# Performance work log

Measured on AMD Instinct MI355X. Metric: run time of the kernel, lower is better.

Reference implementation:

```python
import jax, jax.numpy as jnp
import numpy as np

N = 50000          # num nodes
DEG = 16           # constant out-degree -> edges[:,0] sorted, every node present
E = N * DEG
NODE_IN = 128
NODE_OUT = 64
EDGE_IN = 128
EDGE_OUT = 64      # must equal NODE_OUT for the reshape in the original module


def _xavier_uniform(key, shape):
    fan_in, fan_out = shape[0], shape[1]
    a = np.sqrt(6.0 / (fan_in + fan_out)).astype(np.float32)
    return jax.random.uniform(key, shape, jnp.float32, -a, a)


def setup_inputs() -> dict:
    key = jax.random.key(0)
    k1, k2, k3, k4, k5, k6, k7 = jax.random.split(key, 7)
    node_fts = jax.random.normal(k1, (N, NODE_IN), jnp.float32)
    edge_fts = jax.random.normal(k2, (N, EDGE_IN), jnp.float32)
    # sorted sources with constant degree so unique(src).shape[0] == N and
    # the original's repeat(bincount) trick is equivalent to gather-by-src
    src = jnp.repeat(jnp.arange(N, dtype=jnp.int32), DEG)
    dst = jax.random.randint(k3, (E,), 0, N, dtype=jnp.int32)
    edges = jnp.stack([src, dst], axis=1)  # [E, 2]
    W_node = _xavier_uniform(k4, (NODE_IN, NODE_OUT))
    W_edge = _xavier_uniform(k5, (EDGE_IN, EDGE_OUT))
    a_node = _xavier_uniform(k6, (2 * NODE_OUT, 1))
    a_edge = _xavier_uniform(k7, (NODE_OUT + EDGE_OUT, 1))
    return {"node_fts": node_fts, "edge_fts": edge_fts, "edges": edges,
            "W_node": W_node, "W_edge": W_edge,
            "a_node": a_node, "a_edge": a_edge}


def reference(node_fts, edge_fts, edges, W_node, W_edge, a_node, a_edge):
    src = edges[:, 0]
    h_v = node_fts @ W_node            # [N, NODE_OUT]
    e_v = edge_fts @ W_edge            # [N, EDGE_OUT]

    # gather endpoint features -> [E, 2*NODE_OUT] / [E, NODE_OUT+EDGE_OUT]
    h_pair = h_v[edges].reshape(-1, 2 * NODE_OUT)
    e_pair = e_v[edges].reshape(-1, NODE_OUT + EDGE_OUT)

    leaky = lambda x: jnp.where(x > 0, x, 0.2 * x)
    node_att = leaky((h_pair @ a_node)[:, 0])   # [E]
    edge_att = leaky((e_pair @ a_edge)[:, 0])   # [E]

    node_att = jnp.exp(jnp.clip(node_att, -2.0, 2.0))
    edge_att = jnp.exp(jnp.clip(edge_att, -2.0, 2.0))

    node_sum = jax.ops.segment_sum(node_att, src, num_segments=N)
    edge_sum = jax.ops.segment_sum(edge_att, src, num_segments=N)

    node_att_norm = node_att / node_sum[src]
    edge_att_norm = edge_att / edge_sum[src]

    node_att_var = jnp.var(node_att_norm, ddof=1)  # torch.var is unbiased
    edge_att_var = jnp.var(edge_att_norm, ddof=1)

    node_out = jax.ops.segment_sum(h_pair * node_att_norm[:, None], src, num_segments=N)
    edge_out = jax.ops.segment_sum(e_pair * edge_att_norm[:, None], src, num_segments=N)
    return node_out, edge_out, node_att_var, edge_att_var
```

## Files before the change

### kernel.cpp

```cpp
#include <hip/hip_runtime.h>
#include <hip/hip_bf16.h>

#define NN 50000
#define DEG 16
#define EE (NN*DEG)
#define CHUNKS 3125

typedef unsigned int uint;
typedef __attribute__((ext_vector_type(8))) short bf16x8;
typedef __attribute__((ext_vector_type(4))) float f32x4;

__device__ inline unsigned short f2b(float f){
  uint u = __float_as_uint(f);
  uint r = (u + 0x7FFFu + ((u >> 16) & 1u)) >> 16;
  return (unsigned short)r;
}
__device__ inline float b2f(uint lo16){ return __uint_as_float(lo16 << 16); }

__global__ __launch_bounds__(256) void gemm_mfma_kernel(
    const float* __restrict__ in0, const float* __restrict__ in1,
    const float* __restrict__ W0,  const float* __restrict__ W1,
    const float* __restrict__ a0,  const float* __restrict__ a1,
    unsigned short* __restrict__ hev,
    float* __restrict__ s1ne, float* __restrict__ s2ne)
{
  const int pass = blockIdx.y;
  const float* in   = pass ? in1 : in0;
  const float* W    = pass ? W1  : W0;
  const float* av   = pass ? a1  : a0;

  __shared__ unsigned short Wt[64*128];
  const int tid = threadIdx.x;
  for (int b = tid; b < 1024; b += 256) {
    const int n  = b >> 4;
    const int k0 = (b & 15) * 8;
    uint4 pk;
    unsigned short* ps = (unsigned short*)&pk;
    #pragma unroll
    for (int j = 0; j < 8; j++) ps[j] = f2b(W[(k0 + j)*64 + n]);
    const int byte = n*256 + ((k0*2) ^ ((n & 7) << 4));
    *(uint4*)((char*)Wt + byte) = pk;
  }
  __syncthreads();

  const int wv   = tid >> 6;
  const int lane = tid & 63;
  const int g    = lane >> 4;
  const int c    = lane & 15;

  bf16x8 wfrag[4][4];
  #pragma unroll
  for (int kt = 0; kt < 4; kt++) {
    #pragma unroll
    for (int nt = 0; nt < 4; nt++) {
      const int n  = nt*16 + c;
      const int kb = (kt*32 + g*8) * 2;
      const int byte = n*256 + (kb ^ ((n & 7) << 4));
      wfrag[kt][nt] = *(bf16x8*)((char*)Wt + byte);
    }
  }
  float a1r[4], a2r[4];
  #pragma unroll
  for (int t = 0; t < 4; t++) { a1r[t] = av[t*16 + c]; a2r[t] = av[64 + t*16 + c]; }

  for (int ch = blockIdx.x*4 + wv; ch < CHUNKS; ch += gridDim.x*4) {
    const int r0 = ch * 16;
    const float* rowp = in + (long)(r0 + c)*128 + g*8;
    float4 ald[8];
    #pragma unroll
    for (int kt = 0; kt < 4; kt++) {
      ald[kt*2]   = *(const float4*)(rowp + kt*32);
      ald[kt*2+1] = *(const float4*)(rowp + kt*32 + 4);
    }
    f32x4 acc[4];
    #pragma unroll
    for (int nt = 0; nt < 4; nt++) acc[nt] = (f32x4){0.f, 0.f, 0.f, 0.f};
    #pragma unroll
    for (int kt = 0; kt < 4; kt++) {
      const float4 u = ald[kt*2], w = ald[kt*2+1];
      bf16x8 af;
      af[0] = (short)f2b(u.x); af[1] = (short)f2b(u.y);
      af[2] = (short)f2b(u.z); af[3] = (short)f2b(u.w);
      af[4] = (short)f2b(w.x); af[5] = (short)f2b(w.y);
      af[6] = (short)f2b(w.z); af[7] = (short)f2b(w.w);
      #pragma unroll
      for (int nt = 0; nt < 4; nt++)
        acc[nt] = __builtin_amdgcn_mfma_f32_16x16x32_bf16(af, wfrag[kt][nt], acc[nt], 0, 0, 0);
    }
    float q1v[4], q2v[4];
    #pragma unroll
    for (int v = 0; v < 4; v++) {
      float t1 = 0.f, t2 = 0.f;
      #pragma unroll
      for (int nt = 0; nt < 4; nt++) {
        t1 = fmaf(acc[nt][v], a1r[nt], t1);
        t2 = fmaf(acc[nt][v], a2r[nt], t2);
      }
      #pragma unroll
      for (int off = 1; off < 16; off <<= 1) {
        t1 += __shfl_xor(t1, off);
        t2 += __shfl_xor(t2, off);
      }
      q1v[v] = t1; q2v[v] = t2;
    }
    if (c < 4) {
      const float sv1 = (c==0) ? q1v[0] : (c==1) ? q1v[1] : (c==2) ? q1v[2] : q1v[3];
      const float sv2 = (c==0) ? q2v[0] : (c==1) ? q2v[1] : (c==2) ? q2v[2] : q2v[3];
      const int r = r0 + g*4 + c;
      s1ne[(long)r*2 + pass] = sv1;
      s2ne[(long)r*2 + pass] = sv2;
    }
    #pragma unroll
    for (int nt = 0; nt < 4; nt++) {
      #pragma unroll
      for (int v = 0; v < 4; v++) {
        const long r = r0 + g*4 + v;
        hev[r*128 + pass*64 + nt*16 + c] = f2b(acc[nt][v]);
      }
    }
  }
}

__global__ __launch_bounds__(256) void attn_kernel(
    const uint* __restrict__ hev,
    const float2* __restrict__ s1ne, const float2* __restrict__ s2ne,
    const int* __restrict__ edges,
    float* __restrict__ outp, double* __restrict__ partials)
{
  const int tid  = threadIdx.x;
  const int wv   = tid >> 6;
  const int lane = tid & 63;
  const int j    = lane >> 4;
  const int cc   = lane & 31;
  double a_qn = 0.0, a_qe = 0.0;
  float* node_out = outp;
  float* edge_out = outp + (long)NN*128;
  const int NG = NN/4;
  for (int grp = blockIdx.x*4 + wv; grp < NG; grp += gridDim.x*4) {
    const int i0 = grp*4;
    const int dst = edges[((long)i0*16 + lane)*2 + 1];
    const float2 s1v = s1ne[i0 + j];
    const float2 gsc = s2ne[dst];
    float xn = s1v.x + gsc.x;
    float xe = s1v.y + gsc.y;
    xn = xn > 0.f ? xn : 0.2f*xn;
    xe = xe > 0.f ? xe : 0.2f*xe;
    xn = fminf(fmaxf(xn, -2.f), 2.f);
    xe = fminf(fmaxf(xe, -2.f), 2.f);
    const float an = expf(xn);
    const float ae = expf(xe);
    float sn = an, se = ae;
    #pragma unroll
    for (int off = 1; off < 16; off <<= 1) {
      sn += __shfl_xor(sn, off);
      se += __shfl_xor(se, off);
    }
    const float wn = an / sn;
    const float we = ae / se;
    float rq = wn*wn, re = we*we;
    #pragma unroll
    for (int off = 1; off < 64; off <<= 1) {
      rq += __shfl_xor(rq, off);
      re += __shfl_xor(re, off);
    }
    if (lane == 0) { a_qn += (double)rq; a_qe += (double)re; }
    float acc0[4], acc1[4];
    #pragma unroll
    for (int t = 0; t < 4; t++) { acc0[t] = 0.f; acc1[t] = 0.f; }
    #pragma unroll
    for (int k = 0; k < 64; k++) {
      const int d     = __builtin_amdgcn_readlane(dst, k);
      const float wnk = __uint_as_float(__builtin_amdgcn_readlane(__float_as_uint(wn), k));
      const float wek = __uint_as_float(__builtin_amdgcn_readlane(__float_as_uint(we), k));
      const float wk  = (lane < 32) ? wnk : wek;
      const uint  v   = hev[(long)d*64 + lane];
      acc0[k >> 4] = fmaf(wk, b2f(v & 0xffffu), acc0[k >> 4]);
      acc1[k >> 4] = fmaf(wk, __uint_as_float(v & 0xffff0000u), acc1[k >> 4]);
    }
    #pragma unroll
    for (int t = 0; t < 4; t++) {
      const long i = i0 + t;
      const uint own = hev[i*64 + lane];
      float* base = (lane < 32 ? node_out : edge_out) + i*128 + 2*cc;
      *(float2*)(base)      = make_float2(b2f(own & 0xffffu),
                                          __uint_as_float(own & 0xffff0000u));
      *(float2*)(base + 64) = make_float2(acc0[t], acc1[t]);
    }
  }
  __shared__ double red[4][2];
  if (lane == 0) { red[wv][0] = a_qn; red[wv][1] = a_qe; }
  __syncthreads();
  if (tid == 0) {
    double t0 = 0, t1 = 0;
    #pragma unroll
    for (int w = 0; w < 4; w++) { t0 += red[w][0]; t1 += red[w][1]; }
    double* p = partials + (long)blockIdx.x*2;
    p[0] = t0; p[1] = t1;
  }
}

__global__ __launch_bounds__(256) void finalize_kernel(
    const double* __restrict__ partials, int nparts, float* __restrict__ outp)
{
  const int tid = threadIdx.x;
  double l0 = 0, l1 = 0;
  for (int b = tid; b < nparts; b += 256) {
    l0 += partials[b*2+0]; l1 += partials[b*2+1];
  }
  __shared__ double red[256][2];
  red[tid][0] = l0; red[tid][1] = l1;
  __syncthreads();
  for (int s = 128; s > 0; s >>= 1) {
    if (tid < s) {
      red[tid][0] += red[tid+s][0];
      red[tid][1] += red[tid+s][1];
    }
    __syncthreads();
  }
  if (tid == 0) {
    const double E = (double)EE;
    const double S = (double)NN;
    double varn = (red[0][0] - S*S/E) / (E - 1.0);
    double vare = (red[0][1] - S*S/E) / (E - 1.0);
    outp[(long)NN*256 + 0] = (float)varn;
    outp[(long)NN*256 + 1] = (float)vare;
  }
}

extern "C" void kernel_launch(void* const* d_in, const int* in_sizes, int n_in,
                              void* d_out, int out_size, void* d_ws, size_t ws_size,
                              hipStream_t stream)
{
  const float* node_fts = (const float*)d_in[0];
  const float* edge_fts = (const float*)d_in[1];
  const int*   edges    = (const int*)d_in[2];
  const float* W_node   = (const float*)d_in[3];
  const float* W_edge   = (const float*)d_in[4];
  const float* a_node   = (const float*)d_in[5];
  const float* a_edge   = (const float*)d_in[6];

  char* ws = (char*)d_ws;
  unsigned short* hev = (unsigned short*)(ws);
  float* s1ne = (float*)(ws + 12800000);
  float* s2ne = (float*)(ws + 13200000);
  double* partials = (double*)(ws + 13600000);
  float* outp = (float*)d_out;

  hipLaunchKernelGGL(gemm_mfma_kernel, dim3(391, 2), dim3(256), 0, stream,
                     node_fts, edge_fts, W_node, W_edge, a_node, a_edge,
                     hev, s1ne, s2ne);
  const int AB = 1563;
  hipLaunchKernelGGL(attn_kernel, dim3(AB), dim3(256), 0, stream,
                     (const uint*)hev,
                     (const float2*)s1ne, (const float2*)s2ne,
                     edges, outp, partials);
  hipLaunchKernelGGL(finalize_kernel, dim3(1), dim3(256), 0, stream,
                     partials, AB, outp);
}
```

Before: 72.82 us.

## Vectorize neighbor gather with 16-byte loads and cross-group shuffle reduction

Rewrites the attention aggregation so each lane loads 16 bytes (8 bf16 values) of a neighbor row instead of 4 bytes. Four lane groups each handle a subset of a node's 16 edges, and the partial sums are combined with xor shuffles before lanes 0-15 write float4 outputs. The self-feature copy and the output stores are also widened to float4. The change further swaps the bf16 conversion for the HIP intrinsic and doubles the grid sizes of both kernels, adding shuffle overhead and more blocks in exchange for fewer, wider memory transactions.

```diff
diff --git a/kernel.cpp b/kernel.cpp
--- a/kernel.cpp
+++ b/kernel.cpp
@@ -11,11 +11,10 @@
 typedef __attribute__((ext_vector_type(4))) float f32x4;
 
 __device__ inline unsigned short f2b(float f){
-  uint u = __float_as_uint(f);
-  uint r = (u + 0x7FFFu + ((u >> 16) & 1u)) >> 16;
-  return (unsigned short)r;
+  return __bfloat16_as_ushort(__float2bfloat16(f));
 }
 __device__ inline float b2f(uint lo16){ return __uint_as_float(lo16 << 16); }
+__device__ inline float bhi(uint v){ return __uint_as_float(v & 0xffff0000u); }
 
 __global__ __launch_bounds__(256) void gemm_mfma_kernel(
     const float* __restrict__ in0, const float* __restrict__ in1,
@@ -131,7 +130,7 @@
   const int wv   = tid >> 6;
   const int lane = tid & 63;
   const int j    = lane >> 4;
-  const int cc   = lane & 31;
+  const int cl   = lane & 15;
   double a_qn = 0.0, a_qe = 0.0;
   float* node_out = outp;
   float* edge_out = outp + (long)NN*128;
@@ -164,27 +163,49 @@
       re += __shfl_xor(re, off);
     }
     if (lane == 0) { a_qn += (double)rq; a_qe += (double)re; }
-    float acc0[4], acc1[4];
-    #pragma unroll
-    for (int t = 0; t < 4; t++) { acc0[t] = 0.f; acc1[t] = 0.f; }
-    #pragma unroll
-    for (int k = 0; k < 64; k++) {
-      const int d     = __builtin_amdgcn_readlane(dst, k);
-      const float wnk = __uint_as_float(__builtin_amdgcn_readlane(__float_as_uint(wn), k));
-      const float wek = __uint_as_float(__builtin_amdgcn_readlane(__float_as_uint(we), k));
-      const float wk  = (lane < 32) ? wnk : wek;
-      const uint  v   = hev[(long)d*64 + lane];
-      acc0[k >> 4] = fmaf(wk, b2f(v & 0xffffu), acc0[k >> 4]);
-      acc1[k >> 4] = fmaf(wk, __uint_as_float(v & 0xffff0000u), acc1[k >> 4]);
-    }
+
+    {
+      const uint4 ov = *(const uint4*)(hev + (long)(i0 + j)*64 + cl*4);
+      float* ob = ((cl < 8) ? node_out : edge_out) + (long)(i0 + j)*128 + 8*(cl & 7);
+      *(float4*)(ob)     = make_float4(b2f(ov.x & 0xffffu), bhi(ov.x),
+                                       b2f(ov.y & 0xffffu), bhi(ov.y));
+      *(float4*)(ob + 4) = make_float4(b2f(ov.z & 0xffffu), bhi(ov.z),
+                                       b2f(ov.w & 0xffffu), bhi(ov.w));
+    }
+
     #pragma unroll
     for (int t = 0; t < 4; t++) {
-      const long i = i0 + t;
-      const uint own = hev[i*64 + lane];
-      float* base = (lane < 32 ? node_out : edge_out) + i*128 + 2*cc;
-      *(float2*)(base)      = make_float2(b2f(own & 0xffffu),
-                                          __uint_as_float(own & 0xffff0000u));
-      *(float2*)(base + 64) = make_float2(acc0[t], acc1[t]);
+      float acc[8];
+      #pragma unroll
+      for (int u = 0; u < 8; u++) acc[u] = 0.f;
+      #pragma unroll
+      for (int m = 0; m < 4; m++) {
+        const int sl    = t*16 + m*4 + j;
+        const int d     = __shfl(dst, sl);
+        const float w2n = __shfl(wn, sl);
+        const float w2e = __shfl(we, sl);
+        const float wk  = (cl < 8) ? w2n : w2e;
+        const uint4 v = *(const uint4*)(hev + (long)d*64 + cl*4);
+        acc[0] = fmaf(wk, b2f(v.x & 0xffffu), acc[0]);
+        acc[1] = fmaf(wk, bhi(v.x),           acc[1]);
+        acc[2] = fmaf(wk, b2f(v.y & 0xffffu), acc[2]);
+        acc[3] = fmaf(wk, bhi(v.y),           acc[3]);
+        acc[4] = fmaf(wk, b2f(v.z & 0xffffu), acc[4]);
+        acc[5] = fmaf(wk, bhi(v.z),           acc[5]);
+        acc[6] = fmaf(wk, b2f(v.w & 0xffffu), acc[6]);
+        acc[7] = fmaf(wk, bhi(v.w),           acc[7]);
+      }
+      #pragma unroll
+      for (int u = 0; u < 8; u++) {
+        acc[u] += __shfl_xor(acc[u], 16);
+        acc[u] += __shfl_xor(acc[u], 32);
+      }
+      if (lane < 16) {
+        float* base = ((cl < 8) ? node_out : edge_out)
+                      + (long)(i0 + t)*128 + 64 + 8*(cl & 7);
+        *(float4*)(base)     = make_float4(acc[0], acc[1], acc[2], acc[3]);
+        *(float4*)(base + 4) = make_float4(acc[4], acc[5], acc[6], acc[7]);
+      }
     }
   }
   __shared__ double red[4][2];
@@ -246,10 +267,10 @@
   double* partials = (double*)(ws + 13600000);
   float* outp = (float*)d_out;
 
-  hipLaunchKernelGGL(gemm_mfma_kernel, dim3(391, 2), dim3(256), 0, stream,
+  hipLaunchKernelGGL(gemm_mfma_kernel, dim3(782, 2), dim3(256), 0, stream,
                      node_fts, edge_fts, W_node, W_edge, a_node, a_edge,
                      hev, s1ne, s2ne);
-  const int AB = 1563;
+  const int AB = 3125;
   hipLaunchKernelGGL(attn_kernel, dim3(AB), dim3(256), 0, stream,
                      (const uint*)hev,
                      (const float2*)s1ne, (const float2*)s2ne,
```

After: 81.20 us. +11.5%, slower.
